# Kernel optimization log

Hardware: AMD Instinct MI355X
Metric: run time of the kernel (lower is better)

## Reference

```python
import jax, jax.numpy as jnp
import numpy as np

B, T, D = 2, 2048, 2048
H = 16
D_HEAD = D // H          # 128
D_SUB = D_HEAD // 2      # 64
SCALE = float(np.sqrt(D_SUB))


def setup_inputs() -> dict:
    key = jax.random.key(0)
    ks = jax.random.split(key, 6)
    s = 1.0 / np.sqrt(D)
    return {
        "x": jax.random.normal(ks[0], (B, T, D), dtype=jnp.float32),
        "W_q": jax.random.normal(ks[1], (D, D), dtype=jnp.float32) * s,
        "W_k": jax.random.normal(ks[2], (D, D), dtype=jnp.float32) * s,
        "W_v": jax.random.normal(ks[3], (D, D), dtype=jnp.float32) * s,
        "W_o": jax.random.normal(ks[4], (D, D), dtype=jnp.float32) * s,
        "lambda_param": jnp.full((H,), 0.8, dtype=jnp.float32),
    }


def reference(x, W_q, W_k, W_v, W_o, lambda_param):
    # Linear layers (torch nn.Linear: x @ W.T), reshape to heads
    Q = (x @ W_q.T).reshape(B, T, H, D_HEAD)
    K = (x @ W_k.T).reshape(B, T, H, D_HEAD)
    V = (x @ W_v.T).reshape(B, T, H, D_HEAD)
    # split each head into two sub-heads
    Q1, Q2 = Q[..., :D_SUB], Q[..., D_SUB:2 * D_SUB]
    K1, K2 = K[..., :D_SUB], K[..., D_SUB:2 * D_SUB]
    # dual attention maps: [B, H, T, T]
    attn1 = jnp.einsum('bthd,bshd->bhts', Q1, K1) / SCALE
    attn2 = jnp.einsum('bthd,bshd->bhts', Q2, K2) / SCALE
    A1 = jax.nn.softmax(attn1, axis=-1)
    A2 = jax.nn.softmax(attn2, axis=-1)
    lam = jax.nn.sigmoid(lambda_param)[None, :, None, None]  # [1,H,1,1]
    A_diff = A1 - lam * A2
    # weighted values -> [B, T, H, d_head] -> [B, T, D]
    out = jnp.einsum('bhts,bshd->bthd', A_diff, V).reshape(B, T, D)
    return out @ W_o.T
```

## Files before the change

### kernel.cpp

```cpp
#include <hip/hip_runtime.h>
#include <math.h>

#define B_  2
#define T_  2048
#define D_  2048
#define H_  16
#define DH  128
#define BT  (B_ * T_)

typedef float    f32x4 __attribute__((ext_vector_type(4)));
typedef _Float16 f16x8 __attribute__((ext_vector_type(8)));
typedef __fp16   fp16x2 __attribute__((ext_vector_type(2)));

typedef __attribute__((address_space(1))) const void* gas_t;
typedef __attribute__((address_space(3))) void*       las_t;

__device__ __forceinline__ void gll16(const void* g, void* l) {
    __builtin_amdgcn_global_load_lds((gas_t)g, (las_t)l, 16, 0, 0);
}

__device__ __forceinline__ unsigned short h16bits(float f) {
    union { _Float16 h; unsigned short u; } c; c.h = (_Float16)f; return c.u;
}
__device__ __forceinline__ unsigned pk2h(float a, float b) {
    union { fp16x2 h; unsigned u; } c;
    c.h = __builtin_amdgcn_cvt_pkrtz(a, b);
    return c.u;
}

__global__ __launch_bounds__(256)
void f32_to_f16_multi(const float* __restrict__ s0, _Float16* __restrict__ d0, int n0,
                      const float* __restrict__ s1, _Float16* __restrict__ d1, int n1,
                      const float* __restrict__ s2, _Float16* __restrict__ d2, int n2,
                      const float* __restrict__ s3, _Float16* __restrict__ d3, int n3,
                      const float* __restrict__ s4, _Float16* __restrict__ d4, int n4) {
    const float* s; _Float16* d; int n;
    switch (blockIdx.y) {
        case 0:  s = s0; d = d0; n = n0; break;
        case 1:  s = s1; d = d1; n = n1; break;
        case 2:  s = s2; d = d2; n = n2; break;
        case 3:  s = s3; d = d3; n = n3; break;
        default: s = s4; d = d4; n = n4; break;
    }
    int i = blockIdx.x * 256 + threadIdx.x;
    if (i >= n) return;
    const float4 a = *(const float4*)(s + (size_t)i * 8);
    const float4 b = *(const float4*)(s + (size_t)i * 8 + 4);
    f16x8 o;
    o[0] = (_Float16)a.x; o[1] = (_Float16)a.y; o[2] = (_Float16)a.z; o[3] = (_Float16)a.w;
    o[4] = (_Float16)b.x; o[5] = (_Float16)b.y; o[6] = (_Float16)b.z; o[7] = (_Float16)b.w;
    *(f16x8*)(d + (size_t)i * 8) = o;
}

#define BKK 64

__device__ __forceinline__ void gemm_body(const _Float16* Ab, const _Float16* Bb,
                                          _Float16* As, _Float16* Bs,
                                          f32x4 acc[4][4], int K, int tid,
                                          int c, int g, int wr, int wc) {
    for (int k0 = 0; k0 < K; k0 += BKK) {
        __syncthreads();
        #pragma unroll
        for (int i = 0; i < 4; ++i) {
            gll16(Ab + (size_t)i * 32 * K + k0, &As[(i * 256 + tid) * 8]);
            gll16(Bb + (size_t)i * 32 * K + k0, &Bs[(i * 256 + tid) * 8]);
        }
        __syncthreads();
        #pragma unroll
        for (int kc = 0; kc < 2; ++kc) {
            f16x8 fa[4], fb[4];
            #pragma unroll
            for (int mi = 0; mi < 4; ++mi) {
                const int row = wr * 64 + mi * 16 + c;
                fa[mi] = *(const f16x8*)&As[row * 64 + (((kc * 4 + g) ^ (c & 7)) * 8)];
            }
            #pragma unroll
            for (int ni = 0; ni < 4; ++ni) {
                const int row = wc * 64 + ni * 16 + c;
                fb[ni] = *(const f16x8*)&Bs[row * 64 + (((kc * 4 + g) ^ (c & 7)) * 8)];
            }
            #pragma unroll
            for (int mi = 0; mi < 4; ++mi)
                #pragma unroll
                for (int ni = 0; ni < 4; ++ni)
                    acc[mi][ni] = __builtin_amdgcn_mfma_f32_16x16x32_f16(fa[mi], fb[ni], acc[mi][ni], 0, 0, 0);
        }
    }
}

__global__ __launch_bounds__(256, 3)
void gemm16_qkv(const _Float16* __restrict__ Xh,
                const _Float16* __restrict__ Wq, const _Float16* __restrict__ Wk,
                const _Float16* __restrict__ Wv,
                _Float16* __restrict__ Qh, _Float16* __restrict__ Kh,
                _Float16* __restrict__ Vt, int M, int N, int K, float c1) {
    __shared__ _Float16 As[128 * BKK];
    __shared__ _Float16 Bs[128 * BKK];

    const _Float16* Bg; _Float16* C16; float osc = 1.f; int epi;
    switch (blockIdx.y) {
        case 0:  Bg = Wq; C16 = Qh; osc = c1; epi = 1; break;
        case 1:  Bg = Wk; C16 = Kh; epi = 1; break;
        default: Bg = Wv; C16 = Vt; epi = 2; break;
    }

    const int tid  = threadIdx.x;
    const int lane = tid & 63;
    const int w    = tid >> 6;
    const int wr   = w >> 1, wc = w & 1;
    const int c    = lane & 15, g = lane >> 4;

    const int nwg = gridDim.x;
    const int bid = blockIdx.x;
    const int swz = (bid & 7) * (nwg >> 3) + (bid >> 3);
    const int nb  = N / 128;
    const int bm  = (swz / nb) * 128;
    const int bn  = (swz % nb) * 128;

    const int srow = tid >> 3;
    const int sg   = (tid & 7) ^ (srow & 7);
    const _Float16* Ab = Xh + (size_t)(bm + srow) * K + sg * 8;
    const _Float16* Bb = Bg + (size_t)(bn + srow) * K + sg * 8;

    f32x4 acc[4][4];
    #pragma unroll
    for (int mi = 0; mi < 4; ++mi)
        #pragma unroll
        for (int ni = 0; ni < 4; ++ni)
            #pragma unroll
            for (int r = 0; r < 4; ++r) acc[mi][ni][r] = 0.f;

    gemm_body(Ab, Bb, As, Bs, acc, K, tid, c, g, wr, wc);

    #pragma unroll
    for (int mi = 0; mi < 4; ++mi) {
        #pragma unroll
        for (int ni = 0; ni < 4; ++ni) {
            const int m0 = bm + wr * 64 + mi * 16 + g * 4;
            const int n  = bn + wc * 64 + ni * 16 + c;
            if (epi == 1) {
                #pragma unroll
                for (int r = 0; r < 4; ++r)
                    C16[(size_t)(m0 + r) * N + n] = (_Float16)(acc[mi][ni][r] * osc);
            } else {
                const int bb = m0 >> 11, t = m0 & (T_ - 1);
                ushort4 o;
                o.x = h16bits(acc[mi][ni][0]); o.y = h16bits(acc[mi][ni][1]);
                o.z = h16bits(acc[mi][ni][2]); o.w = h16bits(acc[mi][ni][3]);
                *(ushort4*)&C16[((size_t)bb * D_ + n) * T_ + t] = o;
            }
        }
    }
}

__global__ __launch_bounds__(256, 3)
void gemm16_f32(const _Float16* __restrict__ Ag, const _Float16* __restrict__ Bg,
                float* __restrict__ Cf, int M, int N, int K) {
    __shared__ _Float16 As[128 * BKK];
    __shared__ _Float16 Bs[128 * BKK];

    const int tid  = threadIdx.x;
    const int lane = tid & 63;
    const int w    = tid >> 6;
    const int wr   = w >> 1, wc = w & 1;
    const int c    = lane & 15, g = lane >> 4;

    const int nwg = gridDim.x;
    const int bid = blockIdx.x;
    const int swz = (bid & 7) * (nwg >> 3) + (bid >> 3);
    const int nb  = N / 128;
    const int bm  = (swz / nb) * 128;
    const int bn  = (swz % nb) * 128;

    const int srow = tid >> 3;
    const int sg   = (tid & 7) ^ (srow & 7);
    const _Float16* Ab = Ag + (size_t)(bm + srow) * K + sg * 8;
    const _Float16* Bb = Bg + (size_t)(bn + srow) * K + sg * 8;

    f32x4 acc[4][4];
    #pragma unroll
    for (int mi = 0; mi < 4; ++mi)
        #pragma unroll
        for (int ni = 0; ni < 4; ++ni)
            #pragma unroll
            for (int r = 0; r < 4; ++r) acc[mi][ni][r] = 0.f;

    gemm_body(Ab, Bb, As, Bs, acc, K, tid, c, g, wr, wc);

    #pragma unroll
    for (int mi = 0; mi < 4; ++mi)
        #pragma unroll
        for (int ni = 0; ni < 4; ++ni) {
            const int m0 = bm + wr * 64 + mi * 16 + g * 4;
            const int n  = bn + wc * 64 + ni * 16 + c;
            #pragma unroll
            for (int r = 0; r < 4; ++r)
                Cf[(size_t)(m0 + r) * N + n] = acc[mi][ni][r];
        }
}

#define QB  128
#define KVB 64

__device__ __forceinline__ void softmax_upd(f32x4 s[4], float& l,
                                            unsigned pk[4][2]) {
    float e[4][4];
    #pragma unroll
    for (int mt = 0; mt < 4; ++mt) {
        #pragma unroll
        for (int r = 0; r < 4; ++r) e[mt][r] = exp2f(s[mt][r]);
        pk[mt][0] = pk2h(e[mt][0], e[mt][1]);
        pk[mt][1] = pk2h(e[mt][2], e[mt][3]);
    }
    float tsum = 0.f;
    #pragma unroll
    for (int mt = 0; mt < 4; ++mt)
        #pragma unroll
        for (int r = 0; r < 4; ++r) tsum += e[mt][r];
    l += tsum;
}

__global__ __launch_bounds__(512, 2)
void diff_attn_f16(_Float16* Qh,
                   const _Float16* __restrict__ Kh,
                   const _Float16* __restrict__ Vt,
                   const float* __restrict__ lambda_param) {
    __shared__ __align__(16) char smem[64 * 1024];
    _Float16* ob = (_Float16*)smem;

    const int tid  = threadIdx.x;
    const int lane = tid & 63;
    const int w    = tid >> 6;
    const int qsub = w >> 1;
    const int path = w & 1;
    const int b    = blockIdx.z, h = blockIdx.y;
    const int t0   = blockIdx.x * QB;
    const int c    = lane & 15;
    const int g    = lane >> 4;

    const float lam = 1.f / (1.f + __expf(-lambda_param[h]));

    const int q0 = t0 + qsub * 32;
    const _Float16* Qg = Qh + (size_t)(b * T_ + q0 + c) * D_ + h * DH + path * 64;
    f16x8 qf[2][2];
    #pragma unroll
    for (int qh = 0; qh < 2; ++qh) {
        qf[qh][0] = *(const f16x8*)&Qg[(size_t)qh * 16 * D_ + g * 8];
        qf[qh][1] = *(const f16x8*)&Qg[(size_t)qh * 16 * D_ + 32 + g * 8];
    }

    f32x4 O[2][8];
    #pragma unroll
    for (int qh = 0; qh < 2; ++qh)
        #pragma unroll
        for (int nt = 0; nt < 8; ++nt)
            #pragma unroll
            for (int r = 0; r < 4; ++r) O[qh][nt][r] = 0.f;
    float l[2] = {0.f, 0.f};

    const int kkey = tid >> 4;
    const int kgs  = (tid & 15) ^ (kkey & 7);
    const int vd   = tid >> 3;
    const int vgs  = (tid & 7) ^ (vd & 7);
    const char* kp[2];
    const char* vp[2];
    #pragma unroll
    for (int i = 0; i < 2; ++i) {
        kp[i] = (const char*)(Kh + ((size_t)(b * T_ + i * 32 + kkey)) * D_ + h * DH + kgs * 8);
        vp[i] = (const char*)(Vt + ((size_t)(b * D_ + h * DH + i * 64 + vd)) * T_ + vgs * 8);
    }
    const size_t KADV = (size_t)KVB * D_ * sizeof(_Float16);
    const size_t VADV = (size_t)KVB * sizeof(_Float16);

    auto STAGE = [&](int buf) {
        char* kb_ = smem + (size_t)buf * 16384;
        char* vb_ = smem + 32768 + (size_t)buf * 16384;
        #pragma unroll
        for (int i = 0; i < 2; ++i) {
            gll16(kp[i], kb_ + (size_t)(i * 512 + tid) * 16);
            gll16(vp[i], vb_ + (size_t)(i * 512 + tid) * 16);
            kp[i] += KADV; vp[i] += VADV;
        }
    };

    STAGE(0);

    const int NT = T_ / KVB;
    for (int t = 0; t < NT; ++t) {
        const int cur = t & 1;
        __syncthreads();
        if (t + 1 < NT) STAGE(cur ^ 1);

        const _Float16* k_s = (const _Float16*)(smem + (size_t)cur * 16384);
        const _Float16* v_s = (const _Float16*)(smem + 32768 + (size_t)cur * 16384);

        f32x4 s[2][4];
        #pragma unroll
        for (int qh = 0; qh < 2; ++qh)
            #pragma unroll
            for (int mt = 0; mt < 4; ++mt)
                #pragma unroll
                for (int r = 0; r < 4; ++r) s[qh][mt][r] = 0.f;
        __builtin_amdgcn_s_setprio(1);
        #pragma unroll
        for (int mt = 0; mt < 4; ++mt) {
            const int key  = mt * 16 + c;
            const int krow = key * 128;
            #pragma unroll
            for (int kb = 0; kb < 2; ++kb) {
                const int gp = ((path * 8 + kb * 4 + g) ^ (key & 7)) * 8;
                f16x8 kf = *(const f16x8*)&k_s[krow + gp];
                s[0][mt] = __builtin_amdgcn_mfma_f32_16x16x32_f16(kf, qf[0][kb], s[0][mt], 0, 0, 0);
                s[1][mt] = __builtin_amdgcn_mfma_f32_16x16x32_f16(kf, qf[1][kb], s[1][mt], 0, 0, 0);
            }
        }
        __builtin_amdgcn_s_setprio(0);

        unsigned pk[2][4][2];
        softmax_upd(s[0], l[0], pk[0]);
        softmax_upd(s[1], l[1], pk[1]);

        const int srcA = ((2 * (g & 1)) << 4) | c;
        const int srcB = ((2 * (g & 1) + 1) << 4) | c;
        const bool hiSel = (g & 2) != 0;
        #pragma unroll
        for (int kb = 0; kb < 2; ++kb) {
            f16x8 vf[8];
            #pragma unroll
            for (int nt = 0; nt < 8; ++nt) {
                const int d  = nt * 16 + c;
                const int gp = ((4 * kb + g) ^ (d & 7)) * 8;
                vf[nt] = *(const f16x8*)&v_s[d * 64 + gp];
            }
            #pragma unroll
            for (int qh = 0; qh < 2; ++qh) {
                unsigned u00 = (unsigned)__shfl((int)pk[qh][2 * kb][0], srcA);
                unsigned u10 = (unsigned)__shfl((int)pk[qh][2 * kb + 1][0], srcA);
                unsigned u01 = (unsigned)__shfl((int)pk[qh][2 * kb][1], srcA);
                unsigned u11 = (unsigned)__shfl((int)pk[qh][2 * kb + 1][1], srcA);
                unsigned u02 = (unsigned)__shfl((int)pk[qh][2 * kb][0], srcB);
                unsigned u12 = (unsigned)__shfl((int)pk[qh][2 * kb + 1][0], srcB);
                unsigned u03 = (unsigned)__shfl((int)pk[qh][2 * kb][1], srcB);
                unsigned u13 = (unsigned)__shfl((int)pk[qh][2 * kb + 1][1], srcB);
                union { unsigned u[4]; f16x8 v; } pa;
                pa.u[0] = hiSel ? u10 : u00;
                pa.u[1] = hiSel ? u11 : u01;
                pa.u[2] = hiSel ? u12 : u02;
                pa.u[3] = hiSel ? u13 : u03;
                __builtin_amdgcn_s_setprio(1);
                #pragma unroll
                for (int nt = 0; nt < 8; ++nt)
                    O[qh][nt] = __builtin_amdgcn_mfma_f32_16x16x32_f16(pa.v, vf[nt], O[qh][nt], 0, 0, 0);
                __builtin_amdgcn_s_setprio(0);
            }
        }
    }

    float il[2][4];
    #pragma unroll
    for (int qh = 0; qh < 2; ++qh)
        #pragma unroll
        for (int r = 0; r < 4; ++r) {
            const int src = (g << 2) | r;
            float L = __shfl(l[qh], src)      + __shfl(l[qh], src + 16)
                    + __shfl(l[qh], src + 32) + __shfl(l[qh], src + 48);
            il[qh][r] = (path ? lam : 1.f) / L;
        }

    __syncthreads();
    if (path) {
        _Float16* obp = ob + (size_t)(qsub * 32) * 132;
        #pragma unroll
        for (int qh = 0; qh < 2; ++qh)
            #pragma unroll
            for (int nt = 0; nt < 8; ++nt)
                #pragma unroll
                for (int r = 0; r < 4; ++r)
                    obp[(qh * 16 + g * 4 + r) * 132 + nt * 16 + c] =
                        (_Float16)(O[qh][nt][r] * il[qh][r]);
    }
    __syncthreads();
    if (!path) {
        const _Float16* obp = ob + (size_t)(qsub * 32) * 132;
        const size_t obase = (size_t)(b * T_ + q0) * D_ + h * DH;
        #pragma unroll
        for (int qh = 0; qh < 2; ++qh)
            #pragma unroll
            for (int nt = 0; nt < 8; ++nt)
                #pragma unroll
                for (int r = 0; r < 4; ++r) {
                    float o = O[qh][nt][r] * il[qh][r]
                            - (float)obp[(qh * 16 + g * 4 + r) * 132 + nt * 16 + c];
                    Qh[obase + (size_t)(qh * 16 + g * 4 + r) * D_ + nt * 16 + c] = (_Float16)o;
                }
    }
}

extern "C" void kernel_launch(void* const* d_in, const int* in_sizes, int n_in,
                              void* d_out, int out_size, void* d_ws, size_t ws_size,
                              hipStream_t stream) {
    const float* x    = (const float*)d_in[0];
    const float* W_q  = (const float*)d_in[1];
    const float* W_k  = (const float*)d_in[2];
    const float* W_v  = (const float*)d_in[3];
    const float* W_o  = (const float*)d_in[4];
    const float* lamp = (const float*)d_in[5];
    float* out = (float*)d_out;

    const size_t PL = (size_t)BT * D_;
    const size_t WL = (size_t)D_ * D_;
    _Float16* Xh = (_Float16*)d_ws;
    _Float16* Wq = Xh + PL;
    _Float16* Wk = Wq + WL;
    _Float16* Wv = Wk + WL;
    _Float16* Wo = Wv + WL;
    _Float16* Qh = Wo + WL;
    _Float16* Kh = Qh + PL;
    _Float16* Vt = Kh + PL;

    const float C1 = 0.125f * 1.44269504089f;

    dim3 gc((unsigned)(PL / 8 + 255) / 256, 5);
    f32_to_f16_multi<<<gc, 256, 0, stream>>>(x,   Xh, (int)(PL / 8),
                                             W_q, Wq, (int)(WL / 8),
                                             W_k, Wk, (int)(WL / 8),
                                             W_v, Wv, (int)(WL / 8),
                                             W_o, Wo, (int)(WL / 8));

    dim3 gq(512, 3);
    gemm16_qkv<<<gq, 256, 0, stream>>>(Xh, Wq, Wk, Wv, Qh, Kh, Vt, BT, D_, D_, C1);

    dim3 ga(T_ / QB, H_, B_);
    diff_attn_f16<<<ga, 512, 0, stream>>>(Qh, Kh, Vt, lamp);

    gemm16_f32<<<dim3(512), 256, 0, stream>>>(Qh, Wo, out, BT, D_, D_);
}
```

Measured before the change: 332.4 us.

## Switch attention kernel to 32x32x16 MFMA with permlane32 swap for P reuse

Reworks the differential attention inner loop to use 32x32x16 f16 MFMA tiles instead of 16x16x32. Each wave now covers 32 queries with one accumulator per 32-wide d tile. The exp'd scores are repacked into the PV operand layout with permlane32_swap rather than eight cross-lane shuffles per tile, and the row-sum reduction and epilogue indexing change to match. The aim is to cut shuffle and LDS traffic and raise MFMA efficiency, in exchange for a more intricate register layout whose indexing must be exactly right.

```diff
diff --git a/kernel.cpp b/kernel.cpp
--- a/kernel.cpp
+++ b/kernel.cpp
@@ -8,8 +8,9 @@
 #define DH  128
 #define BT  (B_ * T_)
 
-typedef float    f32x4 __attribute__((ext_vector_type(4)));
-typedef _Float16 f16x8 __attribute__((ext_vector_type(8)));
+typedef float    f32x4  __attribute__((ext_vector_type(4)));
+typedef float    f32x16 __attribute__((ext_vector_type(16)));
+typedef _Float16 f16x8  __attribute__((ext_vector_type(8)));
 typedef __fp16   fp16x2 __attribute__((ext_vector_type(2)));
 
 typedef __attribute__((address_space(1))) const void* gas_t;
@@ -202,24 +203,6 @@
 #define QB  128
 #define KVB 64
 
-__device__ __forceinline__ void softmax_upd(f32x4 s[4], float& l,
-                                            unsigned pk[4][2]) {
-    float e[4][4];
-    #pragma unroll
-    for (int mt = 0; mt < 4; ++mt) {
-        #pragma unroll
-        for (int r = 0; r < 4; ++r) e[mt][r] = exp2f(s[mt][r]);
-        pk[mt][0] = pk2h(e[mt][0], e[mt][1]);
-        pk[mt][1] = pk2h(e[mt][2], e[mt][3]);
-    }
-    float tsum = 0.f;
-    #pragma unroll
-    for (int mt = 0; mt < 4; ++mt)
-        #pragma unroll
-        for (int r = 0; r < 4; ++r) tsum += e[mt][r];
-    l += tsum;
-}
-
 __global__ __launch_bounds__(512, 2)
 void diff_attn_f16(_Float16* Qh,
                    const _Float16* __restrict__ Kh,
@@ -233,30 +216,26 @@
     const int w    = tid >> 6;
     const int qsub = w >> 1;
     const int path = w & 1;
-    const int b    = blockIdx.z, h = blockIdx.y;
+    const int b    = blockIdx.z, hd = blockIdx.y;
     const int t0   = blockIdx.x * QB;
-    const int c    = lane & 15;
-    const int g    = lane >> 4;
-
-    const float lam = 1.f / (1.f + __expf(-lambda_param[h]));
+    const int c32  = lane & 31;
+    const int hh   = lane >> 5;
+
+    const float lam = 1.f / (1.f + __expf(-lambda_param[hd]));
 
     const int q0 = t0 + qsub * 32;
-    const _Float16* Qg = Qh + (size_t)(b * T_ + q0 + c) * D_ + h * DH + path * 64;
-    f16x8 qf[2][2];
-    #pragma unroll
-    for (int qh = 0; qh < 2; ++qh) {
-        qf[qh][0] = *(const f16x8*)&Qg[(size_t)qh * 16 * D_ + g * 8];
-        qf[qh][1] = *(const f16x8*)&Qg[(size_t)qh * 16 * D_ + 32 + g * 8];
-    }
-
-    f32x4 O[2][8];
-    #pragma unroll
-    for (int qh = 0; qh < 2; ++qh)
-        #pragma unroll
-        for (int nt = 0; nt < 8; ++nt)
-            #pragma unroll
-            for (int r = 0; r < 4; ++r) O[qh][nt][r] = 0.f;
-    float l[2] = {0.f, 0.f};
+    const _Float16* Qg = Qh + (size_t)(b * T_ + q0 + c32) * D_ + hd * DH + path * 64;
+    f16x8 qf[4];
+    #pragma unroll
+    for (int ch = 0; ch < 4; ++ch)
+        qf[ch] = *(const f16x8*)&Qg[ch * 16 + hh * 8];
+
+    f32x16 O[4];
+    #pragma unroll
+    for (int dt = 0; dt < 4; ++dt)
+        #pragma unroll
+        for (int r = 0; r < 16; ++r) O[dt][r] = 0.f;
+    float l = 0.f;
 
     const int kkey = tid >> 4;
     const int kgs  = (tid & 15) ^ (kkey & 7);
@@ -266,8 +245,8 @@
     const char* vp[2];
     #pragma unroll
     for (int i = 0; i < 2; ++i) {
-        kp[i] = (const char*)(Kh + ((size_t)(b * T_ + i * 32 + kkey)) * D_ + h * DH + kgs * 8);
-        vp[i] = (const char*)(Vt + ((size_t)(b * D_ + h * DH + i * 64 + vd)) * T_ + vgs * 8);
+        kp[i] = (const char*)(Kh + ((size_t)(b * T_ + i * 32 + kkey)) * D_ + hd * DH + kgs * 8);
+        vp[i] = (const char*)(Vt + ((size_t)(b * D_ + hd * DH + i * 64 + vd)) * T_ + vgs * 8);
     }
     const size_t KADV = (size_t)KVB * D_ * sizeof(_Float16);
     const size_t VADV = (size_t)KVB * sizeof(_Float16);
@@ -294,105 +273,84 @@
         const _Float16* k_s = (const _Float16*)(smem + (size_t)cur * 16384);
         const _Float16* v_s = (const _Float16*)(smem + 32768 + (size_t)cur * 16384);
 
-        f32x4 s[2][4];
-        #pragma unroll
-        for (int qh = 0; qh < 2; ++qh)
-            #pragma unroll
-            for (int mt = 0; mt < 4; ++mt)
-                #pragma unroll
-                for (int r = 0; r < 4; ++r) s[qh][mt][r] = 0.f;
-        __builtin_amdgcn_s_setprio(1);
-        #pragma unroll
-        for (int mt = 0; mt < 4; ++mt) {
-            const int key  = mt * 16 + c;
+        #pragma unroll
+        for (int kt = 0; kt < 2; ++kt) {
+            f32x16 P;
+            #pragma unroll
+            for (int r = 0; r < 16; ++r) P[r] = 0.f;
+            const int key = kt * 32 + c32;
             const int krow = key * 128;
-            #pragma unroll
-            for (int kb = 0; kb < 2; ++kb) {
-                const int gp = ((path * 8 + kb * 4 + g) ^ (key & 7)) * 8;
+            __builtin_amdgcn_s_setprio(1);
+            #pragma unroll
+            for (int ch = 0; ch < 4; ++ch) {
+                const int gp = ((path * 8 + ch * 2 + hh) ^ (key & 7)) * 8;
                 f16x8 kf = *(const f16x8*)&k_s[krow + gp];
-                s[0][mt] = __builtin_amdgcn_mfma_f32_16x16x32_f16(kf, qf[0][kb], s[0][mt], 0, 0, 0);
-                s[1][mt] = __builtin_amdgcn_mfma_f32_16x16x32_f16(kf, qf[1][kb], s[1][mt], 0, 0, 0);
-            }
-        }
-        __builtin_amdgcn_s_setprio(0);
-
-        unsigned pk[2][4][2];
-        softmax_upd(s[0], l[0], pk[0]);
-        softmax_upd(s[1], l[1], pk[1]);
-
-        const int srcA = ((2 * (g & 1)) << 4) | c;
-        const int srcB = ((2 * (g & 1) + 1) << 4) | c;
-        const bool hiSel = (g & 2) != 0;
-        #pragma unroll
-        for (int kb = 0; kb < 2; ++kb) {
-            f16x8 vf[8];
-            #pragma unroll
-            for (int nt = 0; nt < 8; ++nt) {
-                const int d  = nt * 16 + c;
-                const int gp = ((4 * kb + g) ^ (d & 7)) * 8;
-                vf[nt] = *(const f16x8*)&v_s[d * 64 + gp];
-            }
-            #pragma unroll
-            for (int qh = 0; qh < 2; ++qh) {
-                unsigned u00 = (unsigned)__shfl((int)pk[qh][2 * kb][0], srcA);
-                unsigned u10 = (unsigned)__shfl((int)pk[qh][2 * kb + 1][0], srcA);
-                unsigned u01 = (unsigned)__shfl((int)pk[qh][2 * kb][1], srcA);
-                unsigned u11 = (unsigned)__shfl((int)pk[qh][2 * kb + 1][1], srcA);
-                unsigned u02 = (unsigned)__shfl((int)pk[qh][2 * kb][0], srcB);
-                unsigned u12 = (unsigned)__shfl((int)pk[qh][2 * kb + 1][0], srcB);
-                unsigned u03 = (unsigned)__shfl((int)pk[qh][2 * kb][1], srcB);
-                unsigned u13 = (unsigned)__shfl((int)pk[qh][2 * kb + 1][1], srcB);
+                P = __builtin_amdgcn_mfma_f32_32x32x16_f16(kf, qf[ch], P, 0, 0, 0);
+            }
+            __builtin_amdgcn_s_setprio(0);
+
+            float e[16];
+            #pragma unroll
+            for (int r = 0; r < 16; ++r) { e[r] = exp2f(P[r]); l += e[r]; }
+
+            #pragma unroll
+            for (int ch2 = 0; ch2 < 2; ++ch2) {
+                unsigned Au = pk2h(e[ch2 * 8 + 0], e[ch2 * 8 + 1]);
+                unsigned Bu = pk2h(e[ch2 * 8 + 2], e[ch2 * 8 + 3]);
+                unsigned Cu = pk2h(e[ch2 * 8 + 4], e[ch2 * 8 + 5]);
+                unsigned Du = pk2h(e[ch2 * 8 + 6], e[ch2 * 8 + 7]);
+                auto rAC = __builtin_amdgcn_permlane32_swap(Au, Cu, false, false);
+                auto rBD = __builtin_amdgcn_permlane32_swap(Bu, Du, false, false);
                 union { unsigned u[4]; f16x8 v; } pa;
-                pa.u[0] = hiSel ? u10 : u00;
-                pa.u[1] = hiSel ? u11 : u01;
-                pa.u[2] = hiSel ? u12 : u02;
-                pa.u[3] = hiSel ? u13 : u03;
+                pa.u[0] = rAC[0]; pa.u[1] = rBD[0];
+                pa.u[2] = rAC[1]; pa.u[3] = rBD[1];
+
+                const int gv = kt * 4 + ch2 * 2 + hh;
                 __builtin_amdgcn_s_setprio(1);
                 #pragma unroll
-                for (int nt = 0; nt < 8; ++nt)
-                    O[qh][nt] = __builtin_amdgcn_mfma_f32_16x16x32_f16(pa.v, vf[nt], O[qh][nt], 0, 0, 0);
+                for (int dt = 0; dt < 4; ++dt) {
+                    const int d = dt * 32 + c32;
+                    f16x8 vf = *(const f16x8*)&v_s[d * 64 + ((gv ^ (d & 7)) * 8)];
+                    O[dt] = __builtin_amdgcn_mfma_f32_32x32x16_f16(pa.v, vf, O[dt], 0, 0, 0);
+                }
                 __builtin_amdgcn_s_setprio(0);
             }
         }
     }
 
-    float il[2][4];
-    #pragma unroll
-    for (int qh = 0; qh < 2; ++qh)
-        #pragma unroll
-        for (int r = 0; r < 4; ++r) {
-            const int src = (g << 2) | r;
-            float L = __shfl(l[qh], src)      + __shfl(l[qh], src + 16)
-                    + __shfl(l[qh], src + 32) + __shfl(l[qh], src + 48);
-            il[qh][r] = (path ? lam : 1.f) / L;
-        }
+    const float lt = l + __shfl_xor(l, 32);
+    const float rl = (path ? lam : 1.f) / lt;
+    float il[16];
+    #pragma unroll
+    for (int r = 0; r < 16; ++r) {
+        const int q = (r & 3) + 8 * (r >> 2) + 4 * hh;
+        il[r] = __shfl(rl, q);
+    }
 
     __syncthreads();
     if (path) {
         _Float16* obp = ob + (size_t)(qsub * 32) * 132;
         #pragma unroll
-        for (int qh = 0; qh < 2; ++qh)
-            #pragma unroll
-            for (int nt = 0; nt < 8; ++nt)
-                #pragma unroll
-                for (int r = 0; r < 4; ++r)
-                    obp[(qh * 16 + g * 4 + r) * 132 + nt * 16 + c] =
-                        (_Float16)(O[qh][nt][r] * il[qh][r]);
+        for (int dt = 0; dt < 4; ++dt)
+            #pragma unroll
+            for (int r = 0; r < 16; ++r) {
+                const int q = (r & 3) + 8 * (r >> 2) + 4 * hh;
+                obp[q * 132 + dt * 32 + c32] = (_Float16)(O[dt][r] * il[r]);
+            }
     }
     __syncthreads();
     if (!path) {
         const _Float16* obp = ob + (size_t)(qsub * 32) * 132;
-        const size_t obase = (size_t)(b * T_ + q0) * D_ + h * DH;
-        #pragma unroll
-        for (int qh = 0; qh < 2; ++qh)
-            #pragma unroll
-            for (int nt = 0; nt < 8; ++nt)
-                #pragma unroll
-                for (int r = 0; r < 4; ++r) {
-                    float o = O[qh][nt][r] * il[qh][r]
-                            - (float)obp[(qh * 16 + g * 4 + r) * 132 + nt * 16 + c];
-                    Qh[obase + (size_t)(qh * 16 + g * 4 + r) * D_ + nt * 16 + c] = (_Float16)o;
-                }
+        const size_t obase = (size_t)(b * T_ + q0) * D_ + hd * DH;
+        #pragma unroll
+        for (int dt = 0; dt < 4; ++dt)
+            #pragma unroll
+            for (int r = 0; r < 16; ++r) {
+                const int q = (r & 3) + 8 * (r >> 2) + 4 * hh;
+                float o = O[dt][r] * il[r]
+                        - (float)obp[q * 132 + dt * 32 + c32];
+                Qh[obase + (size_t)q * D_ + dt * 32 + c32] = (_Float16)o;
+            }
     }
 }
 
```

Measured after the change: 321.3 us. -3.4%, faster.
